# Optimization experiments

Hardware: AMD Instinct MI355X
Metric: run time of the kernel (lower is better)

The kernel has to match this reference:

```python
import jax, jax.numpy as jnp
import numpy as np

TAU = 0.5  # routing_temperature


def setup_inputs() -> dict:
    key = jax.random.key(0)
    ks = jax.random.split(key, 12)
    B, N, D = 8, 4096, 384  # d_inner = 384, grid 64x64
    G = 4
    s = 0.02
    inp = {
        "x": jax.random.normal(ks[0], (B, N, D), dtype=jnp.float32),
        "W_stream1": jax.random.normal(ks[1], (D, D), dtype=jnp.float32) * s,
        "b_stream1": jnp.zeros((D,), dtype=jnp.float32),
        "W_stream2": jax.random.normal(ks[2], (D, G), dtype=jnp.float32) * s,
        "b_stream2": jnp.zeros((G,), dtype=jnp.float32),
        "self_bias": jnp.full((1, G, 1, 1), 2.0, dtype=jnp.float32),
        "W_ga": jax.random.normal(ks[3], (D, D), dtype=jnp.float32) * s,
        "b_ga": jnp.full((D,), 1.5, dtype=jnp.float32),
        "W_gb": jax.random.normal(ks[4], (D, D), dtype=jnp.float32) * s,
        "b_gb": jnp.full((D,), -1.5, dtype=jnp.float32),
        "W_inj": jax.random.normal(ks[5], (D, 2 * D), dtype=jnp.float32) * s,
        "W_state": jax.random.normal(ks[6], (D, 2 * D), dtype=jnp.float32) * s,
        "W_out": jax.random.normal(ks[7], (2 * D, D), dtype=jnp.float32) * s,
        "D_skip": jnp.ones((D,), dtype=jnp.float32),
        "k_steps": 4,
    }
    return inp


def reference(x, W_stream1, b_stream1, W_stream2, b_stream2, self_bias,
              W_ga, b_ga, W_gb, b_gb, W_inj, W_state, W_out, D_skip, k_steps):
    B, N, D = x.shape
    h = w = int(round(N ** 0.5))
    G = self_bias.shape[1]
    C = D // G

    def to_grid(t):  # (B, N, F) -> (B, F, h, w)
        return jnp.transpose(t, (0, 2, 1)).reshape(B, -1, h, w)

    # state (U, V)
    uv = x @ W_state
    u, v = jnp.split(uv, 2, axis=-1)
    u, v = to_grid(u), to_grid(v)

    # stream function -> divergence-free velocity (discrete curl)
    psi = to_grid(jax.nn.silu(x @ W_stream1 + b_stream1) @ W_stream2 + b_stream2)
    psi_h = jnp.pad(psi, ((0, 0), (0, 0), (1, 1), (0, 0)))
    vx = 0.5 * (psi_h[:, :, 2:, :] - psi_h[:, :, :-2, :])
    psi_w = jnp.pad(psi, ((0, 0), (0, 0), (0, 0), (1, 1)))
    vy = -0.5 * (psi_w[:, :, :, 2:] - psi_w[:, :, :, :-2])

    # 5-neighbor routing: [self, up, down, left, right]
    logits = jnp.stack([
        jnp.broadcast_to(self_bias, vx.shape),
        -vx / TAU, vx / TAU, -vy / TAU, vy / TAU,
    ], axis=2)  # (B, G, 5, h, w)
    routing = jax.nn.softmax(logits, axis=2)

    gate_a = to_grid(jax.nn.sigmoid(x @ W_ga + b_ga))
    gate_b = to_grid(jax.nn.sigmoid(x @ W_gb + b_gb))

    inj = x @ W_inj
    xu, xv = jnp.split(inj, 2, axis=-1)
    xu, xv = to_grid(xu), to_grid(xv)

    def transport(state):  # (B, D, h, w)
        sp_h = jnp.pad(state, ((0, 0), (0, 0), (1, 1), (0, 0)))
        s_up, s_down = sp_h[:, :, :-2, :], sp_h[:, :, 2:, :]
        sp_w = jnp.pad(state, ((0, 0), (0, 0), (0, 0), (1, 1)))
        s_left, s_right = sp_w[:, :, :, :-2], sp_w[:, :, :, 2:]
        nb = jnp.stack([state, s_up, s_down, s_left, s_right], axis=2)  # (B,D,5,h,w)
        nb = nb.reshape(B, G, C, 5, h, w)
        out = jnp.einsum('bgcnhw,bgnhw->bgchw', nb, routing)
        return out.reshape(B, D, h, w)

    for _ in range(int(k_steps)):
        u = gate_a * transport(u) + gate_b * xu
        v = gate_a * transport(v) + gate_b * xv

    u_out = jnp.transpose(u.reshape(B, D, N), (0, 2, 1))
    v_out = jnp.transpose(v.reshape(B, D, N), (0, 2, 1))
    combined = jnp.concatenate([u_out, v_out], axis=-1)
    return combined @ W_out + x * D_skip
```

## Files before the change

### kernel.cpp

```cpp
#include <hip/hip_runtime.h>
#include <hip/hip_bf16.h>

typedef __attribute__((ext_vector_type(8))) short bf16x8;
typedef __attribute__((ext_vector_type(4))) short short4v;
typedef __attribute__((ext_vector_type(4))) float f32x4;

#define TAU_INV 2.0f

__device__ __forceinline__ short f2bf(float f) {
  unsigned u = __float_as_uint(f);
  u += 0x7fffu + ((u >> 16) & 1u);
  return (short)(u >> 16);
}
__device__ __forceinline__ float bf2f(short s) {
  return __uint_as_float(((unsigned)(unsigned short)s) << 16);
}

__global__ __launch_bounds__(256) void prep_weights(
    const float* __restrict__ w_state, const float* __restrict__ w_inj,
    const float* __restrict__ w_ga, const float* __restrict__ w_gb,
    const float* __restrict__ w_s1, const float* __restrict__ w_out,
    short* __restrict__ t_cat, short* __restrict__ t_out)
{
  int idx = blockIdx.x * 256 + threadIdx.x;
  const int NCAT = 2688 * 384;
  if (idx < NCAT) {
    int c = idx / 384, k = idx - c * 384;
    float v;
    if (c < 768)        v = w_state[k * 768 + c];
    else if (c < 1536)  v = w_inj[k * 768 + (c - 768)];
    else if (c < 1920)  v = w_ga[k * 384 + (c - 1536)];
    else if (c < 2304)  v = w_gb[k * 384 + (c - 1920)];
    else                v = w_s1[k * 384 + (c - 2304)];
    t_cat[idx] = f2bf(v);
  } else {
    int j = idx - NCAT;
    int c = j / 768, k = j - c * 768;
    t_out[c * 768 + k] = f2bf(w_out[k * 384 + c]);
  }
}

__global__ __launch_bounds__(256) void prep_x(
    const float* __restrict__ X, short* __restrict__ Xb)
{
  int t = blockIdx.x * 256 + threadIdx.x;
  int base = t * 8;
  float4 a = *(const float4*)(X + base);
  float4 b = *(const float4*)(X + base + 4);
  bf16x8 s;
  s[0] = f2bf(a.x); s[1] = f2bf(a.y); s[2] = f2bf(a.z); s[3] = f2bf(a.w);
  s[4] = f2bf(b.x); s[5] = f2bf(b.y); s[6] = f2bf(b.z); s[7] = f2bf(b.w);
  *(bf16x8*)(Xb + base) = s;
}

__global__ __launch_bounds__(256) void gemm_fused(
    const short* __restrict__ Xb, const short* __restrict__ Wt,
    const float* __restrict__ b_ga, const float* __restrict__ b_gb,
    const float* __restrict__ b_s1,
    short* __restrict__ ug, short* __restrict__ vg,
    short* __restrict__ xug, short* __restrict__ xvg,
    short* __restrict__ gag, short* __restrict__ gbg,
    short* __restrict__ s1)
{
  __shared__ short As[128 * 72];
  __shared__ short Bs[128 * 72];
  const int tid = threadIdx.x;
  const int lane = tid & 63;
  const int wv = tid >> 6;
  const int wr = wv >> 1, wc = wv & 1;
  const int m0 = blockIdx.x * 128, c0 = blockIdx.y * 128;
  const int l15 = lane & 15, l4 = lane >> 4;
  f32x4 acc[4][4] = {};
  for (int k0 = 0; k0 < 384; k0 += 64) {
    __syncthreads();
#pragma unroll
    for (int i = 0; i < 4; ++i) {
      int h = tid + i * 256;
      int m = h >> 3, kc = (h & 7) * 8;
      bf16x8 xv = *(const bf16x8*)(Xb + (m0 + m) * 384 + k0 + kc);
      *(bf16x8*)(As + m * 72 + kc) = xv;
    }
#pragma unroll
    for (int i = 0; i < 4; ++i) {
      int h = tid + i * 256;
      int c = h >> 3, kc = (h & 7) * 8;
      bf16x8 wvv = *(const bf16x8*)(Wt + (c0 + c) * 384 + k0 + kc);
      *(bf16x8*)(Bs + c * 72 + kc) = wvv;
    }
    __syncthreads();
#pragma unroll
    for (int kk = 0; kk < 2; ++kk) {
      bf16x8 af[4], bfv[4];
#pragma unroll
      for (int f = 0; f < 4; ++f) {
        af[f]  = *(const bf16x8*)(As + (wr * 64 + f * 16 + l15) * 72 + kk * 32 + l4 * 8);
        bfv[f] = *(const bf16x8*)(Bs + (wc * 64 + f * 16 + l15) * 72 + kk * 32 + l4 * 8);
      }
#pragma unroll
      for (int i = 0; i < 4; ++i)
#pragma unroll
        for (int j = 0; j < 4; ++j)
          acc[i][j] = __builtin_amdgcn_mfma_f32_16x16x32_bf16(af[i], bfv[j], acc[i][j], 0, 0, 0);
    }
  }
#pragma unroll
  for (int i = 0; i < 4; ++i) {
#pragma unroll
    for (int j = 0; j < 4; ++j) {
      const int c = c0 + wc * 64 + j * 16 + l15;
      const int mb = m0 + wr * 64 + i * 16 + l4 * 4;
      const int b = mb >> 12, n = mb & 4095;
      f32x4 v = acc[i][j];
      if (c < 1536) {
        int cc = (c >= 768) ? (c - 768) : c;
        short* base;
        if (c < 768) base = (cc < 384) ? ug : vg;
        else         base = (cc < 384) ? xug : xvg;
        int plane = (cc >= 384) ? (cc - 384) : cc;
        short4v s;
        s[0] = f2bf(v[0]); s[1] = f2bf(v[1]); s[2] = f2bf(v[2]); s[3] = f2bf(v[3]);
        *(short4v*)(base + (b * 384 + plane) * 4096 + n) = s;
      } else if (c < 2304) {
        const float* bias = (c < 1920) ? b_ga : b_gb;
        short* base = (c < 1920) ? gag : gbg;
        int plane = (c < 1920) ? (c - 1536) : (c - 1920);
        float bb = bias[plane];
        short4v s;
#pragma unroll
        for (int r = 0; r < 4; ++r) {
          float t = v[r] + bb;
          s[r] = f2bf(1.f / (1.f + __expf(-t)));
        }
        *(short4v*)(base + (b * 384 + plane) * 4096 + n) = s;
      } else {
        int plane = c - 2304;
        float bb = b_s1[plane];
#pragma unroll
        for (int r = 0; r < 4; ++r) {
          float t = v[r] + bb;
          float sg = 1.f / (1.f + __expf(-t));
          s1[(mb + r) * 384 + plane] = f2bf(t * sg);
        }
      }
    }
  }
}

__global__ __launch_bounds__(256) void psi_kernel(
    const short* __restrict__ S1, const float* __restrict__ W2,
    const float* __restrict__ b2, float* __restrict__ psi)
{
  const int lane = threadIdx.x & 63;
  const int wv = threadIdx.x >> 6;
  const int m = blockIdx.x * 4 + wv;
  float a0 = 0.f, a1 = 0.f, a2 = 0.f, a3 = 0.f;
#pragma unroll
  for (int t = 0; t < 6; ++t) {
    int k = lane + t * 64;
    float sv = bf2f(S1[m * 384 + k]);
    float4 wr = *(const float4*)(W2 + k * 4);
    a0 += sv * wr.x; a1 += sv * wr.y; a2 += sv * wr.z; a3 += sv * wr.w;
  }
  for (int off = 32; off > 0; off >>= 1) {
    a0 += __shfl_down(a0, off, 64);
    a1 += __shfl_down(a1, off, 64);
    a2 += __shfl_down(a2, off, 64);
    a3 += __shfl_down(a3, off, 64);
  }
  if (lane == 0) {
    int bb = m >> 12, n = m & 4095;
    psi[(bb * 4 + 0) * 4096 + n] = a0 + b2[0];
    psi[(bb * 4 + 1) * 4096 + n] = a1 + b2[1];
    psi[(bb * 4 + 2) * 4096 + n] = a2 + b2[2];
    psi[(bb * 4 + 3) * 4096 + n] = a3 + b2[3];
  }
}

__global__ __launch_bounds__(256) void routing_kernel(
    const float* __restrict__ psi, const float* __restrict__ sb,
    float* __restrict__ R)
{
  const int idx = blockIdx.x * 256 + threadIdx.x;
  const int n = idx & 4095, bg = idx >> 12;
  const int i = n >> 6, j = n & 63;
  const float* p = psi + bg * 4096;
  float up = (i > 0)  ? p[n - 64] : 0.f;
  float dn = (i < 63) ? p[n + 64] : 0.f;
  float lf = (j > 0)  ? p[n - 1]  : 0.f;
  float rt = (j < 63) ? p[n + 1]  : 0.f;
  float vx = 0.5f * (dn - up);
  float vy = -0.5f * (rt - lf);
  float l0 = sb[bg & 3];
  float l1 = -vx * TAU_INV, l2 = vx * TAU_INV, l3 = -vy * TAU_INV, l4v = vy * TAU_INV;
  float mx = fmaxf(fmaxf(fmaxf(l0, l1), fmaxf(l2, l3)), l4v);
  float e0 = __expf(l0 - mx), e1 = __expf(l1 - mx), e2 = __expf(l2 - mx);
  float e3 = __expf(l3 - mx), e4 = __expf(l4v - mx);
  float inv = 1.f / (e0 + e1 + e2 + e3 + e4);
  const int NP = 8 * 4 * 4096;
  R[0 * NP + idx] = e0 * inv;
  R[1 * NP + idx] = e1 * inv;
  R[2 * NP + idx] = e2 * inv;
  R[3 * NP + idx] = e3 * inv;
  R[4 * NP + idx] = e4 * inv;
}

__global__ __launch_bounds__(512, 4) void transport_kernel(
    short* __restrict__ Ug, short* __restrict__ Vg,
    const short* __restrict__ Ga, const short* __restrict__ Gb,
    const short* __restrict__ Xu, const short* __restrict__ Xv,
    const float* __restrict__ R, const int* __restrict__ ksp)
{
  __shared__ float sm[64 * 65];
  const int tid = threadIdx.x;
  const int bid = blockIdx.x;
  const int uv = bid & 1;
  const int bd = bid >> 1;
  const int b = bd / 384;
  const int d = bd - b * 384;
  const int g = d / 96;
  short* __restrict__ S = uv ? Vg : Ug;
  const short* __restrict__ Xi = uv ? Xv : Xu;
  const int pbase = bd * 4096;
  const int rbase = (b * 4 + g) * 4096;
  const int NP = 8 * 4 * 4096;
  const int p0 = tid * 8;
  const int i = tid >> 3;
  const int j0 = (tid & 7) * 8;
  const int base = i * 65 + j0;

  float ar0[8], ar1[8], ar2[8], ar3[8], ar4[8], bx[8];
  {
    float ga[8];
    bf16x8 t;
    t = *(const bf16x8*)(Ga + pbase + p0);
#pragma unroll
    for (int c = 0; c < 8; ++c) ga[c] = bf2f(t[c]);
    t = *(const bf16x8*)(Gb + pbase + p0);
    bf16x8 tx = *(const bf16x8*)(Xi + pbase + p0);
#pragma unroll
    for (int c = 0; c < 8; ++c) bx[c] = bf2f(t[c]) * bf2f(tx[c]);
#pragma unroll
    for (int q = 0; q < 2; ++q) {
      float4 f0 = *(const float4*)(R + 0 * NP + rbase + p0 + q * 4);
      float4 f1 = *(const float4*)(R + 1 * NP + rbase + p0 + q * 4);
      float4 f2 = *(const float4*)(R + 2 * NP + rbase + p0 + q * 4);
      float4 f3 = *(const float4*)(R + 3 * NP + rbase + p0 + q * 4);
      float4 f4 = *(const float4*)(R + 4 * NP + rbase + p0 + q * 4);
      ar0[q*4+0]=ga[q*4+0]*f0.x; ar0[q*4+1]=ga[q*4+1]*f0.y; ar0[q*4+2]=ga[q*4+2]*f0.z; ar0[q*4+3]=ga[q*4+3]*f0.w;
      ar1[q*4+0]=ga[q*4+0]*f1.x; ar1[q*4+1]=ga[q*4+1]*f1.y; ar1[q*4+2]=ga[q*4+2]*f1.z; ar1[q*4+3]=ga[q*4+3]*f1.w;
      ar2[q*4+0]=ga[q*4+0]*f2.x; ar2[q*4+1]=ga[q*4+1]*f2.y; ar2[q*4+2]=ga[q*4+2]*f2.z; ar2[q*4+3]=ga[q*4+3]*f2.w;
      ar3[q*4+0]=ga[q*4+0]*f3.x; ar3[q*4+1]=ga[q*4+1]*f3.y; ar3[q*4+2]=ga[q*4+2]*f3.z; ar3[q*4+3]=ga[q*4+3]*f3.w;
      ar4[q*4+0]=ga[q*4+0]*f4.x; ar4[q*4+1]=ga[q*4+1]*f4.y; ar4[q*4+2]=ga[q*4+2]*f4.z; ar4[q*4+3]=ga[q*4+3]*f4.w;
    }
    bf16x8 ts = *(const bf16x8*)(S + pbase + p0);
#pragma unroll
    for (int c = 0; c < 8; ++c) sm[base + c] = bf2f(ts[c]);
  }
  __syncthreads();
  const int ks = ksp[0];
  const bool hasUp = (i > 0), hasDn = (i < 63);
  for (int step = 0; step < ks; ++step) {
    float cu[8], nu[8];
#pragma unroll
    for (int c = 0; c < 8; ++c) cu[c] = sm[base + c];
    float lfe = (j0 > 0)  ? sm[base - 1] : 0.f;
    float rte = (j0 < 56) ? sm[base + 8] : 0.f;
#pragma unroll
    for (int c = 0; c < 8; ++c) {
      float up = hasUp ? sm[base - 65 + c] : 0.f;
      float dn = hasDn ? sm[base + 65 + c] : 0.f;
      float lf = (c > 0) ? cu[c - 1] : lfe;
      float rt = (c < 7) ? cu[c + 1] : rte;
      nu[c] = ar0[c]*cu[c] + ar1[c]*up + ar2[c]*dn + ar3[c]*lf + ar4[c]*rt + bx[c];
    }
    __syncthreads();
#pragma unroll
    for (int c = 0; c < 8; ++c) sm[base + c] = nu[c];
    __syncthreads();
  }
  bf16x8 os;
#pragma unroll
  for (int c = 0; c < 8; ++c) os[c] = f2bf(sm[base + c]);
  *(bf16x8*)(S + pbase + p0) = os;
}

__global__ __launch_bounds__(256) void gemm_final(
    const short* __restrict__ U, const short* __restrict__ V,
    const short* __restrict__ Wt, const float* __restrict__ X,
    const float* __restrict__ Dskip, float* __restrict__ out)
{
  __shared__ short As[64 * 128];
  __shared__ short Bs[128 * 72];
  const int tid = threadIdx.x;
  const int lane = tid & 63;
  const int wv = tid >> 6, wr = wv >> 1, wc = wv & 1;
  const int m0 = blockIdx.x * 128, c0 = blockIdx.y * 128;
  const int b = m0 >> 12, n0 = m0 & 4095;
  const int l15 = lane & 15, l4 = lane >> 4;
  f32x4 acc[4][4] = {};
  for (int k0 = 0; k0 < 768; k0 += 64) {
    const short* src = (k0 < 384) ? U : V;
    const int kp = (k0 >= 384) ? (k0 - 384) : k0;
    __syncthreads();
#pragma unroll
    for (int i = 0; i < 4; ++i) {
      int h = tid + i * 256;
      int k = h >> 4, cc = h & 15;
      bf16x8 tv = *(const bf16x8*)(src + (b * 384 + kp + k) * 4096 + n0 + cc * 8);
      int ccs = cc ^ (((k >> 3) & 3) << 1);
      *(bf16x8*)(As + k * 128 + ccs * 8) = tv;
    }
#pragma unroll
    for (int i = 0; i < 4; ++i) {
      int h = tid + i * 256;
      int c = h >> 3, kc = (h & 7) * 8;
      bf16x8 wvv = *(const bf16x8*)(Wt + (c0 + c) * 768 + k0 + kc);
      *(bf16x8*)(Bs + c * 72 + kc) = wvv;
    }
    __syncthreads();
#pragma unroll
    for (int kk = 0; kk < 2; ++kk) {
      bf16x8 af[4], bfv[4];
#pragma unroll
      for (int f = 0; f < 4; ++f) {
        const int mm = wr * 64 + f * 16 + l15;
        const int chunk = mm >> 3, wi = mm & 7;
        bf16x8 av;
#pragma unroll
        for (int jj = 0; jj < 8; ++jj) {
          int k = kk * 32 + l4 * 8 + jj;
          int ccs = chunk ^ (((k >> 3) & 3) << 1);
          av[jj] = As[k * 128 + ccs * 8 + wi];
        }
        af[f] = av;
        bfv[f] = *(const bf16x8*)(Bs + (wc * 64 + f * 16 + l15) * 72 + kk * 32 + l4 * 8);
      }
#pragma unroll
      for (int i = 0; i < 4; ++i)
#pragma unroll
        for (int j = 0; j < 4; ++j)
          acc[i][j] = __builtin_amdgcn_mfma_f32_16x16x32_bf16(af[i], bfv[j], acc[i][j], 0, 0, 0);
    }
  }
#pragma unroll
  for (int i = 0; i < 4; ++i)
#pragma unroll
    for (int j = 0; j < 4; ++j) {
      const int c = c0 + wc * 64 + j * 16 + l15;
      const int mb = m0 + wr * 64 + i * 16 + l4 * 4;
      const float ds = Dskip[c];
#pragma unroll
      for (int r = 0; r < 4; ++r) {
        int idx = (mb + r) * 384 + c;
        out[idx] = acc[i][j][r] + X[idx] * ds;
      }
    }
}

extern "C" void kernel_launch(void* const* d_in, const int* in_sizes, int n_in,
                              void* d_out, int out_size, void* d_ws, size_t ws_size,
                              hipStream_t stream) {
  (void)in_sizes; (void)n_in; (void)out_size; (void)ws_size;
  const float* x       = (const float*)d_in[0];
  const float* w_s1    = (const float*)d_in[1];
  const float* b_s1    = (const float*)d_in[2];
  const float* w_s2    = (const float*)d_in[3];
  const float* b_s2    = (const float*)d_in[4];
  const float* sb      = (const float*)d_in[5];
  const float* w_ga    = (const float*)d_in[6];
  const float* b_ga    = (const float*)d_in[7];
  const float* w_gb    = (const float*)d_in[8];
  const float* b_gb    = (const float*)d_in[9];
  const float* w_inj   = (const float*)d_in[10];
  const float* w_state = (const float*)d_in[11];
  const float* w_out   = (const float*)d_in[12];
  const float* dskip   = (const float*)d_in[13];
  const int*   ksp     = (const int*)d_in[14];
  float* out = (float*)d_out;

  char* ws = (char*)d_ws;
  size_t off = 0;
  auto alloc = [&](size_t bytes) -> void* {
    void* p = ws + off;
    off += (bytes + 255) & ~(size_t)255;
    return p;
  };
  short* t_cat = (short*)alloc((size_t)2688 * 384 * 2);
  short* t_out = (short*)alloc((size_t)384 * 768 * 2);
  const size_t PL = (size_t)8 * 384 * 4096;
  short* xb  = (short*)alloc(PL * 2);
  short* ug  = (short*)alloc(PL * 2);
  short* vg  = (short*)alloc(PL * 2);
  short* xug = (short*)alloc(PL * 2);
  short* xvg = (short*)alloc(PL * 2);
  short* gag = (short*)alloc(PL * 2);
  short* gbg = (short*)alloc(PL * 2);
  short* s1  = (short*)alloc(PL * 2);
  float* psi = (float*)alloc((size_t)8 * 4 * 4096 * 4);
  float* R   = (float*)alloc((size_t)5 * 8 * 4 * 4096 * 4);

  prep_weights<<<dim3(5184), dim3(256), 0, stream>>>(
      w_state, w_inj, w_ga, w_gb, w_s1, w_out, t_cat, t_out);
  prep_x<<<dim3(6144), dim3(256), 0, stream>>>(x, xb);
  gemm_fused<<<dim3(256, 21), dim3(256), 0, stream>>>(
      xb, t_cat, b_ga, b_gb, b_s1, ug, vg, xug, xvg, gag, gbg, s1);
  psi_kernel<<<dim3(8192), dim3(256), 0, stream>>>(s1, w_s2, b_s2, psi);
  routing_kernel<<<dim3(512), dim3(256), 0, stream>>>(psi, sb, R);
  transport_kernel<<<dim3(6144), dim3(512), 0, stream>>>(ug, vg, gag, gbg, xug, xvg, R, ksp);
  gemm_final<<<dim3(256, 3), dim3(256), 0, stream>>>(ug, vg, t_out, x, dskip, out);
}
```

Measured before the change: 412.6 us.

## Pre-tile and XOR-swizzle GEMM operands, load tiles directly into LDS

After: 391.2 us. 1.05x faster.

```diff
diff --git a/kernel.cpp b/kernel.cpp
--- a/kernel.cpp
+++ b/kernel.cpp
@@ -15,6 +15,7 @@
 __device__ __forceinline__ float bf2f(short s) {
   return __uint_as_float(((unsigned)(unsigned short)s) << 16);
 }
+
 
 __global__ __launch_bounds__(256) void prep_weights(
     const float* __restrict__ w_state, const float* __restrict__ w_inj,
@@ -23,9 +24,16 @@
     short* __restrict__ t_cat, short* __restrict__ t_out)
 {
   int idx = blockIdx.x * 256 + threadIdx.x;
-  const int NCAT = 2688 * 384;
+  const int NCAT = 21 * 6 * 8192;
   if (idx < NCAT) {
-    int c = idx / 384, k = idx - c * 384;
+    int tile = idx >> 13;
+    int o = idx & 8191;
+    int ct = tile / 6, kt = tile - ct * 6;
+    int r = o >> 6;
+    int s = (o >> 3) & 7;
+    int e = o & 7;
+    int c = ct * 128 + r;
+    int k = kt * 64 + ((s ^ (r & 7)) << 3) + e;
     float v;
     if (c < 768)        v = w_state[k * 768 + c];
     else if (c < 1536)  v = w_inj[k * 768 + (c - 768)];
@@ -41,20 +49,26 @@
 }
 
 __global__ __launch_bounds__(256) void prep_x(
-    const float* __restrict__ X, short* __restrict__ Xb)
+    const float* __restrict__ X, short* __restrict__ XbT)
 {
   int t = blockIdx.x * 256 + threadIdx.x;
-  int base = t * 8;
-  float4 a = *(const float4*)(X + base);
-  float4 b = *(const float4*)(X + base + 4);
-  bf16x8 s;
-  s[0] = f2bf(a.x); s[1] = f2bf(a.y); s[2] = f2bf(a.z); s[3] = f2bf(a.w);
-  s[4] = f2bf(b.x); s[5] = f2bf(b.y); s[6] = f2bf(b.z); s[7] = f2bf(b.w);
-  *(bf16x8*)(Xb + base) = s;
+  int tile = t >> 10;
+  int o = t & 1023;
+  int mt = tile / 6, kt = tile - mt * 6;
+  int r = o >> 3, s = o & 7;
+  int m = mt * 128 + r;
+  int k = kt * 64 + ((s ^ (r & 7)) << 3);
+  const float* src = X + m * 384 + k;
+  float4 a = *(const float4*)(src);
+  float4 b = *(const float4*)(src + 4);
+  bf16x8 sv;
+  sv[0] = f2bf(a.x); sv[1] = f2bf(a.y); sv[2] = f2bf(a.z); sv[3] = f2bf(a.w);
+  sv[4] = f2bf(b.x); sv[5] = f2bf(b.y); sv[6] = f2bf(b.z); sv[7] = f2bf(b.w);
+  *(bf16x8*)(XbT + (size_t)t * 8) = sv;
 }
 
 __global__ __launch_bounds__(256) void gemm_fused(
-    const short* __restrict__ Xb, const short* __restrict__ Wt,
+    const short* __restrict__ XbT, const short* __restrict__ WtT,
     const float* __restrict__ b_ga, const float* __restrict__ b_gb,
     const float* __restrict__ b_s1,
     short* __restrict__ ug, short* __restrict__ vg,
@@ -62,39 +76,42 @@
     short* __restrict__ gag, short* __restrict__ gbg,
     short* __restrict__ s1)
 {
-  __shared__ short As[128 * 72];
-  __shared__ short Bs[128 * 72];
+  __shared__ __align__(16) short As[8192];
+  __shared__ __align__(16) short Bs[8192];
   const int tid = threadIdx.x;
-  const int lane = tid & 63;
+  const int ln = tid & 63;
   const int wv = tid >> 6;
   const int wr = wv >> 1, wc = wv & 1;
-  const int m0 = blockIdx.x * 128, c0 = blockIdx.y * 128;
-  const int l15 = lane & 15, l4 = lane >> 4;
+  const int mt = blockIdx.x, ct = blockIdx.y;
+  const int l15 = ln & 15, l4 = ln >> 4;
+  const int lsw = l15 & 7;
   f32x4 acc[4][4] = {};
-  for (int k0 = 0; k0 < 384; k0 += 64) {
-    __syncthreads();
+  const short* aSrc = XbT + (size_t)(mt * 6) * 8192 + wv * 2048 + ln * 8;
+  const short* bSrc = WtT + (size_t)(ct * 6) * 8192 + wv * 2048 + ln * 8;
+  for (int kt = 0; kt < 6; ++kt) {
 #pragma unroll
     for (int i = 0; i < 4; ++i) {
-      int h = tid + i * 256;
-      int m = h >> 3, kc = (h & 7) * 8;
-      bf16x8 xv = *(const bf16x8*)(Xb + (m0 + m) * 384 + k0 + kc);
-      *(bf16x8*)(As + m * 72 + kc) = xv;
-    }
-#pragma unroll
-    for (int i = 0; i < 4; ++i) {
-      int h = tid + i * 256;
-      int c = h >> 3, kc = (h & 7) * 8;
-      bf16x8 wvv = *(const bf16x8*)(Wt + (c0 + c) * 384 + k0 + kc);
-      *(bf16x8*)(Bs + c * 72 + kc) = wvv;
-    }
+      __builtin_amdgcn_global_load_lds(
+          (const __attribute__((address_space(1))) void*)(aSrc + i * 512),
+          (__attribute__((address_space(3))) void*)(As + (wv * 4 + i) * 512),
+          16, 0, 0);
+      __builtin_amdgcn_global_load_lds(
+          (const __attribute__((address_space(1))) void*)(bSrc + i * 512),
+          (__attribute__((address_space(3))) void*)(Bs + (wv * 4 + i) * 512),
+          16, 0, 0);
+    }
+    aSrc += 8192; bSrc += 8192;
     __syncthreads();
 #pragma unroll
     for (int kk = 0; kk < 2; ++kk) {
       bf16x8 af[4], bfv[4];
 #pragma unroll
       for (int f = 0; f < 4; ++f) {
-        af[f]  = *(const bf16x8*)(As + (wr * 64 + f * 16 + l15) * 72 + kk * 32 + l4 * 8);
-        bfv[f] = *(const bf16x8*)(Bs + (wc * 64 + f * 16 + l15) * 72 + kk * 32 + l4 * 8);
+        const int ra = wr * 64 + f * 16 + l15;
+        const int rb = wc * 64 + f * 16 + l15;
+        const int sl = (((kk << 2) | l4) ^ lsw) << 3;
+        af[f]  = *(const bf16x8*)(As + ra * 64 + sl);
+        bfv[f] = *(const bf16x8*)(Bs + rb * 64 + sl);
       }
 #pragma unroll
       for (int i = 0; i < 4; ++i)
@@ -102,7 +119,9 @@
         for (int j = 0; j < 4; ++j)
           acc[i][j] = __builtin_amdgcn_mfma_f32_16x16x32_bf16(af[i], bfv[j], acc[i][j], 0, 0, 0);
     }
-  }
+    __syncthreads();
+  }
+  const int m0 = mt * 128, c0 = ct * 128;
 #pragma unroll
   for (int i = 0; i < 4; ++i) {
 #pragma unroll
@@ -385,10 +404,10 @@
     off += (bytes + 255) & ~(size_t)255;
     return p;
   };
-  short* t_cat = (short*)alloc((size_t)2688 * 384 * 2);
+  short* t_cat = (short*)alloc((size_t)21 * 6 * 8192 * 2);
   short* t_out = (short*)alloc((size_t)384 * 768 * 2);
   const size_t PL = (size_t)8 * 384 * 4096;
-  short* xb  = (short*)alloc(PL * 2);
+  short* xbt = (short*)alloc(PL * 2);
   short* ug  = (short*)alloc(PL * 2);
   short* vg  = (short*)alloc(PL * 2);
   short* xug = (short*)alloc(PL * 2);
@@ -401,9 +420,9 @@
 
   prep_weights<<<dim3(5184), dim3(256), 0, stream>>>(
       w_state, w_inj, w_ga, w_gb, w_s1, w_out, t_cat, t_out);
-  prep_x<<<dim3(6144), dim3(256), 0, stream>>>(x, xb);
+  prep_x<<<dim3(6144), dim3(256), 0, stream>>>(x, xbt);
   gemm_fused<<<dim3(256, 21), dim3(256), 0, stream>>>(
-      xb, t_cat, b_ga, b_gb, b_s1, ug, vg, xug, xvg, gag, gbg, s1);
+      xbt, t_cat, b_ga, b_gb, b_s1, ug, vg, xug, xvg, gag, gbg, s1);
   psi_kernel<<<dim3(8192), dim3(256), 0, stream>>>(s1, w_s2, b_s2, psi);
   routing_kernel<<<dim3(512), dim3(256), 0, stream>>>(psi, sb, R);
   transport_kernel<<<dim3(6144), dim3(512), 0, stream>>>(ug, vg, gag, gbg, xug, xvg, R, ksp);
```
